# Kernel optimization log

Measured on AMD Instinct MI355X. Metric: run time of the kernel, lower is better.

## Reference

```python
import jax, jax.numpy as jnp
import numpy as np

U = 8001   # n_users + 1
I = 16001  # n_items + 1
B = 8192


def setup_inputs() -> dict:
    key = jax.random.key(0)
    ks = jax.random.split(key, 5)
    rating_mtx = jax.random.uniform(ks[0], (U, I), dtype=jnp.float32) * 5.0
    mask = jax.random.uniform(ks[1], (U, I)) < 0.2
    rating_mtx = jnp.where(mask, rating_mtx, 0.0)
    user_similarity = jax.random.normal(ks[2], (U, U), dtype=jnp.float32) * (2.0 / (U + U)) ** 0.5
    user = jax.random.randint(ks[3], (B,), 0, U)
    item = jax.random.randint(ks[4], (B,), 0, I)
    nz = rating_mtx > 0
    global_bias = jnp.sum(jnp.where(nz, rating_mtx, 0.0)) / jnp.sum(nz)
    return {
        "user": user,
        "item": item,
        "rating_mtx": rating_mtx,
        "user_similarity": user_similarity,
        "user_bias": jnp.zeros((U,), jnp.float32),
        "item_bias": jnp.zeros((I,), jnp.float32),
        "global_bias": global_bias.astype(jnp.float32),
    }


def compute_user_bias(rating_mtx):
    # fused masked mean per user row over nonzero entries
    nz = rating_mtx != 0
    s = jnp.sum(jnp.where(nz, rating_mtx, 0.0), axis=1)
    c = jnp.sum(nz, axis=1).astype(rating_mtx.dtype)
    return jnp.where(c > 0, s / jnp.maximum(c, 1.0), 0.0)


def reference(user, item, rating_mtx, user_similarity, user_bias, item_bias, global_bias):
    ub_fixed = compute_user_bias(rating_mtx)                 # [U]
    adjusted = rating_mtx - ub_fixed[:, None]                # [U, I]
    similarities = user_similarity[user]                     # [B, U]
    item_ratings = adjusted[:, item]                         # [U, B]
    user_scores = jnp.einsum('bu,ub->b', similarities, item_ratings)
    bias = user_bias[user] + item_bias[item] + global_bias
    pred = user_scores + bias
    return jax.nn.sigmoid(pred) * 5.0
```

## Files before the change

kernel.cpp:

```cpp
#include <hip/hip_runtime.h>
#include <math.h>

#define U_DIM 8001
#define I_DIM 16001
#define B_DIM 8192

__device__ __forceinline__ unsigned short f32_to_bf16_rne(float f) {
    union { float f; unsigned int u; } v; v.f = f;
    unsigned int r = v.u + 0x7fffu + ((v.u >> 16) & 1u);
    return (unsigned short)(r >> 16);
}
__device__ __forceinline__ float bf16_to_f32(unsigned short h) {
    union { unsigned int u; float f; } v; v.u = ((unsigned int)h) << 16;
    return v.f;
}

__global__ __launch_bounds__(1024)
void gather_kernel(const float* __restrict__ R, const int* __restrict__ item,
                   unsigned short* __restrict__ Ag, int row0) {
    __shared__ float rowbuf[I_DIM];
    __shared__ float red_s[16];
    __shared__ int   red_c[16];

    const int u   = row0 + blockIdx.x;
    const int tid = threadIdx.x;
    const float* rp = R + (size_t)u * I_DIM;

    float s = 0.f; int c = 0;
    const int pre  = (4 - (u & 3)) & 3;
    const int nvec = (I_DIM - pre) >> 2;
    const int vend = pre + (nvec << 2);

    for (int i = tid; i < pre; i += 1024) {
        float v = rp[i]; rowbuf[i] = v; s += v; c += (v != 0.f);
    }
    const float4* rv = (const float4*)(rp + pre);
    for (int i = tid; i < nvec; i += 1024) {
        float4 v = rv[i];
        const int base = pre + (i << 2);
        rowbuf[base    ] = v.x;
        rowbuf[base + 1] = v.y;
        rowbuf[base + 2] = v.z;
        rowbuf[base + 3] = v.w;
        s += v.x + v.y + v.z + v.w;
        c += (v.x != 0.f) + (v.y != 0.f) + (v.z != 0.f) + (v.w != 0.f);
    }
    for (int i = vend + tid; i < I_DIM; i += 1024) {
        float v = rp[i]; rowbuf[i] = v; s += v; c += (v != 0.f);
    }

    #pragma unroll
    for (int off = 32; off > 0; off >>= 1) {
        s += __shfl_down(s, off, 64);
        c += __shfl_down(c, off, 64);
    }
    const int wid  = tid >> 6;
    const int lane = tid & 63;
    if (lane == 0) { red_s[wid] = s; red_c[wid] = c; }
    __syncthreads();

    float Sr = 0.f; int Cr = 0;
    #pragma unroll
    for (int k = 0; k < 16; ++k) { Sr += red_s[k]; Cr += red_c[k]; }
    const float ub = (Cr > 0) ? Sr / (float)Cr : 0.f;

    unsigned short* arow = Ag + (size_t)blockIdx.x * B_DIM;
    for (int b = tid; b < B_DIM; b += 1024) {
        float ad = rowbuf[item[b]] - ub;
        __builtin_nontemporal_store(f32_to_bf16_rne(ad), &arow[b]);
    }
}

__global__ __launch_bounds__(256)
void dot2_kernel(const float* __restrict__ S, const int* __restrict__ user,
                 const unsigned short* __restrict__ Ag, float* __restrict__ accum,
                 int row0, int nrows, int uchunk) {
    const int b   = blockIdx.x * 256 + threadIdx.x;
    const int usr = user[b];
    const float* srow = S + (size_t)usr * U_DIM + row0;

    const int ulo = blockIdx.y * uchunk;
    const int uhi = min(nrows, ulo + uchunk);

    float acc = 0.f;
    #pragma unroll 4
    for (int r = ulo; r < uhi; ++r) {
        unsigned short h = __builtin_nontemporal_load(&Ag[(size_t)r * B_DIM + b]);
        acc += srow[r] * bf16_to_f32(h);
    }
    atomicAdd(&accum[b], acc);
}

__global__ void finish_kernel(const float* __restrict__ accum,
                              const int* __restrict__ user,
                              const int* __restrict__ item,
                              const float* __restrict__ ubias,
                              const float* __restrict__ ibias,
                              const float* __restrict__ gb,
                              float* __restrict__ out) {
    const int b = blockIdx.x * blockDim.x + threadIdx.x;
    if (b < B_DIM) {
        float pred = accum[b] + ubias[user[b]] + ibias[item[b]] + gb[0];
        out[b] = 5.f / (1.f + expf(-pred));
    }
}

extern "C" void kernel_launch(void* const* d_in, const int* in_sizes, int n_in,
                              void* d_out, int out_size, void* d_ws, size_t ws_size,
                              hipStream_t stream) {
    const int*   user = (const int*)  d_in[0];
    const int*   item = (const int*)  d_in[1];
    const float* R    = (const float*)d_in[2];
    const float* S    = (const float*)d_in[3];
    const float* ubia = (const float*)d_in[4];
    const float* ibia = (const float*)d_in[5];
    const float* gb   = (const float*)d_in[6];
    float* out   = (float*)d_out;

    float*          accum = (float*)d_ws;
    unsigned short* Ag    = (unsigned short*)((char*)d_ws + (size_t)B_DIM * 4);

    size_t rg_bytes = (ws_size > (size_t)B_DIM * 4) ? ws_size - (size_t)B_DIM * 4 : 0;
    int max_rows = (int)(rg_bytes / ((size_t)B_DIM * 2));
    if (max_rows > U_DIM) max_rows = U_DIM;
    if (max_rows < 1)     max_rows = 1;

    hipMemsetAsync(accum, 0, B_DIM * sizeof(float), stream);

    for (int row0 = 0; row0 < U_DIM; row0 += max_rows) {
        const int nrows = min(max_rows, U_DIM - row0);
        gather_kernel<<<nrows, 1024, 0, stream>>>(R, item, Ag, row0);
        const int uchunk = 250;
        const int nuc = (nrows + uchunk - 1) / uchunk;
        dot2_kernel<<<dim3(B_DIM / 256, nuc), 256, 0, stream>>>(S, user, Ag, accum,
                                                                row0, nrows, uchunk);
    }

    finish_kernel<<<(B_DIM + 255) / 256, 256, 0, stream>>>(accum, user, item,
                                                           ubia, ibia, gb, out);
}
```

Measured before the change: 928.4 us.

## Stage similarity rows in LDS with coalesced loads for dot kernel

The dot kernel is restructured so each block handles 64 batch entries. Each block cooperatively loads contiguous chunks of their similarity rows into XOR-swizzled shared memory, replacing the strided per-thread reads of S where every thread walked a different row. The four waves split the rows, and the result is accumulated with atomics. The gather kernel also marks its rating-matrix loads as nontemporal. The new layout adds barriers and shared-memory traffic per chunk, and each block now covers only 64 lanes of Ag, so Ag reads are less wide.

```diff
diff --git a/kernel.cpp b/kernel.cpp
--- a/kernel.cpp
+++ b/kernel.cpp
@@ -4,6 +4,11 @@
 #define U_DIM 8001
 #define I_DIM 16001
 #define B_DIM 8192
+#define BTILE 64
+#define RC    128
+#define NYSPLIT 16
+
+typedef float f32x4 __attribute__((ext_vector_type(4)));
 
 __device__ __forceinline__ unsigned short f32_to_bf16_rne(float f) {
     union { float f; unsigned int u; } v; v.f = f;
@@ -34,16 +39,16 @@
     for (int i = tid; i < pre; i += 1024) {
         float v = rp[i]; rowbuf[i] = v; s += v; c += (v != 0.f);
     }
-    const float4* rv = (const float4*)(rp + pre);
+    const f32x4* rv = (const f32x4*)(rp + pre);
     for (int i = tid; i < nvec; i += 1024) {
-        float4 v = rv[i];
+        f32x4 v = __builtin_nontemporal_load(rv + i);
         const int base = pre + (i << 2);
-        rowbuf[base    ] = v.x;
-        rowbuf[base + 1] = v.y;
-        rowbuf[base + 2] = v.z;
-        rowbuf[base + 3] = v.w;
-        s += v.x + v.y + v.z + v.w;
-        c += (v.x != 0.f) + (v.y != 0.f) + (v.z != 0.f) + (v.w != 0.f);
+        rowbuf[base    ] = v[0];
+        rowbuf[base + 1] = v[1];
+        rowbuf[base + 2] = v[2];
+        rowbuf[base + 3] = v[3];
+        s += v[0] + v[1] + v[2] + v[3];
+        c += (v[0] != 0.f) + (v[1] != 0.f) + (v[2] != 0.f) + (v[3] != 0.f);
     }
     for (int i = vend + tid; i < I_DIM; i += 1024) {
         float v = rp[i]; rowbuf[i] = v; s += v; c += (v != 0.f);
@@ -72,23 +77,50 @@
 }
 
 __global__ __launch_bounds__(256)
-void dot2_kernel(const float* __restrict__ S, const int* __restrict__ user,
+void dot3_kernel(const float* __restrict__ S, const int* __restrict__ user,
                  const unsigned short* __restrict__ Ag, float* __restrict__ accum,
-                 int row0, int nrows, int uchunk) {
-    const int b   = blockIdx.x * 256 + threadIdx.x;
-    const int usr = user[b];
-    const float* srow = S + (size_t)usr * U_DIM + row0;
+                 int row0, int nrows) {
+    __shared__ float s_lds[BTILE][RC];
+    __shared__ int   usr_s[BTILE];
 
-    const int ulo = blockIdx.y * uchunk;
-    const int uhi = min(nrows, ulo + uchunk);
+    const int tid  = threadIdx.x;
+    const int lane = tid & 63;
+    const int w    = tid >> 6;
+    const int b0   = blockIdx.x * BTILE;
+
+    const int rpy = (nrows + NYSPLIT - 1) / NYSPLIT;
+    const int rlo = blockIdx.y * rpy;
+    const int rhi = min(nrows, rlo + rpy);
+
+    if (tid < BTILE) usr_s[tid] = user[b0 + tid];
+    __syncthreads();
 
     float acc = 0.f;
-    #pragma unroll 4
-    for (int r = ulo; r < uhi; ++r) {
-        unsigned short h = __builtin_nontemporal_load(&Ag[(size_t)r * B_DIM + b]);
-        acc += srow[r] * bf16_to_f32(h);
+    const unsigned short* agb = Ag + b0 + lane;
+    const int sw = lane & 31;
+
+    for (int r0 = rlo; r0 < rhi; r0 += RC) {
+        const int rc = min(RC, rhi - r0);
+
+        #pragma unroll
+        for (int k = 0; k < 16; ++k) {
+            const int row = (w << 4) + k;
+            const float* sp = S + (size_t)usr_s[row] * U_DIM + row0 + r0;
+            for (int i = lane; i < rc; i += 64)
+                s_lds[row][i ^ (row & 31)] = sp[i];
+        }
+        __syncthreads();
+
+        const unsigned short* agp = agb + (size_t)r0 * B_DIM;
+        #pragma unroll 8
+        for (int rr = w; rr < rc; rr += 4) {
+            unsigned short h = __builtin_nontemporal_load(agp + (size_t)rr * B_DIM);
+            acc += s_lds[lane][rr ^ sw] * bf16_to_f32(h);
+        }
+        __syncthreads();
     }
-    atomicAdd(&accum[b], acc);
+
+    atomicAdd(&accum[b0 + lane], acc);
 }
 
 __global__ void finish_kernel(const float* __restrict__ accum,
@@ -130,10 +162,8 @@
     for (int row0 = 0; row0 < U_DIM; row0 += max_rows) {
         const int nrows = min(max_rows, U_DIM - row0);
         gather_kernel<<<nrows, 1024, 0, stream>>>(R, item, Ag, row0);
-        const int uchunk = 250;
-        const int nuc = (nrows + uchunk - 1) / uchunk;
-        dot2_kernel<<<dim3(B_DIM / 256, nuc), 256, 0, stream>>>(S, user, Ag, accum,
-                                                                row0, nrows, uchunk);
+        dot3_kernel<<<dim3(B_DIM / BTILE, NYSPLIT), 256, 0, stream>>>(
+            S, user, Ag, accum, row0, nrows);
     }
 
     finish_kernel<<<(B_DIM + 255) / 256, 256, 0, stream>>>(accum, user, item,
```

New measurement: 912.7 us. About the same (-1.7%).
